# Performance work log

Measured on AMD Instinct MI355X. Metric: run time of the kernel, lower is better.

Reference implementation:

```python
import jax, jax.numpy as jnp
import numpy as np

B, C, M = 8192, 1024, 4096  # batch, controller width, memory_size


def setup_inputs() -> dict:
    key = jax.random.key(0)
    k1, k2, k3 = jax.random.split(key, 3)
    memory = jax.random.normal(k1, (B, M), dtype=jnp.float32)
    controller_output = jax.random.normal(k2, (B, C), dtype=jnp.float32)
    W = jax.random.normal(k3, (C, M), dtype=jnp.float32) * 0.02  # Dense kernel
    b = jnp.zeros((M,), dtype=jnp.float32)                       # Dense bias
    return {"memory": memory, "controller_output": controller_output, "W": W, "b": b}


def _l2_normalize(x, eps=1e-12):
    # matches tf.linalg.l2_normalize: x / sqrt(max(sum(x^2), eps))
    return x / jnp.sqrt(jnp.maximum(jnp.sum(x * x, axis=-1, keepdims=True), eps))


def reference(memory, controller_output, W, b):
    # Dense key projection followed by softmax over memory width
    key_vec = jax.nn.softmax(controller_output @ W + b, axis=-1)        # [B, M]
    # tf.keras.losses.cosine_similarity = -sum(l2n(a) * l2n(b), -1)
    sims = -jnp.sum(_l2_normalize(key_vec) * _l2_normalize(memory), axis=-1)  # [B]
    read_weights = jax.nn.softmax(sims, axis=-1)                        # softmax over B (as in source)
    read_vector = jnp.sum(read_weights[:, None] * memory, axis=1)       # [B]
    return read_vector
```

## Files before the change

kernel.cpp:

```cpp
#include <hip/hip_runtime.h>

#define NB 8192
#define NC 1024
#define NM 4096
#define NCH 16

typedef __attribute__((ext_vector_type(8))) short bf16x8;
typedef __attribute__((ext_vector_type(4))) float f32x4;

__device__ __forceinline__ unsigned short f2bf(float x) {
  unsigned int u = __float_as_uint(x);
  u += 0x7FFFu + ((u >> 16) & 1u);
  return (unsigned short)(u >> 16);
}
__device__ __forceinline__ float bf2f(unsigned short h) {
  return __uint_as_float(((unsigned int)h) << 16);
}
__device__ __forceinline__ unsigned int pk2(float a, float b) {
  return (unsigned int)f2bf(a) | ((unsigned int)f2bf(b) << 16);
}

__device__ __forceinline__ void gload_lds16(const void* g, void* l) {
  __builtin_amdgcn_global_load_lds(
      (const __attribute__((address_space(1))) unsigned int*)g,
      (__attribute__((address_space(3))) unsigned int*)l, 16, 0, 0);
}

#define DSR(dst, addr, IMM) \
  asm volatile("ds_read_b128 %0, %1 offset:" IMM : "=v"(dst) : "v"(addr))

#define BAR asm volatile("s_barrier" ::: "memory")
#define SBAR __builtin_amdgcn_sched_barrier(0)

__global__ __launch_bounds__(256) void prep_k(const float* __restrict__ W,
                                              unsigned short* __restrict__ Wt,
                                              const float* __restrict__ coin,
                                              unsigned short* __restrict__ Abf) {
  __shared__ float tile[64][65];
  const int bid = blockIdx.x;
  const int t = threadIdx.x;
  if (bid < 1024) {
    const int n0 = (bid & 63) * 64, k0 = (bid >> 6) * 64;
    const int r = t >> 2, q = t & 3;
    const float4* src = reinterpret_cast<const float4*>(W + (size_t)(k0 + r) * NM + n0 + q * 16);
    float4 x0 = src[0], x1 = src[1], x2 = src[2], x3 = src[3];
    float* tr = &tile[r][q * 16];
    tr[0]=x0.x; tr[1]=x0.y; tr[2]=x0.z;  tr[3]=x0.w;
    tr[4]=x1.x; tr[5]=x1.y; tr[6]=x1.z;  tr[7]=x1.w;
    tr[8]=x2.x; tr[9]=x2.y; tr[10]=x2.z; tr[11]=x2.w;
    tr[12]=x3.x; tr[13]=x3.y; tr[14]=x3.z; tr[15]=x3.w;
    __syncthreads();
    unsigned int pk[8];
#pragma unroll
    for (int i = 0; i < 8; ++i)
      pk[i] = pk2(tile[q * 16 + 2 * i][r], tile[q * 16 + 2 * i + 1][r]);
    int4* dst = reinterpret_cast<int4*>(Wt + (size_t)(n0 + r) * NC + k0 + q * 16);
    dst[0] = make_int4((int)pk[0], (int)pk[1], (int)pk[2], (int)pk[3]);
    dst[1] = make_int4((int)pk[4], (int)pk[5], (int)pk[6], (int)pk[7]);
  } else {
    const size_t i = ((size_t)(bid - 1024) * 256 + t) * 8;
    const float4* s = reinterpret_cast<const float4*>(coin + i);
    float4 x0 = s[0], x1 = s[1];
    int4 o = make_int4((int)pk2(x0.x, x0.y), (int)pk2(x0.z, x0.w),
                       (int)pk2(x1.x, x1.y), (int)pk2(x1.z, x1.w));
    *reinterpret_cast<int4*>(Abf + i) = o;
  }
}

__global__ __launch_bounds__(512) void gemm_fused(
    const unsigned short* __restrict__ Abf, const float* __restrict__ memry,
    const unsigned short* __restrict__ Wt, const float* __restrict__ bvec,
    float* __restrict__ pdotg, float* __restrict__ pesqg,
    float* __restrict__ pmsqg, float* __restrict__ pmsg) {
  __shared__ __align__(16) unsigned short LDS[2][4][8192];
  const int bm = blockIdx.x, bn = blockIdx.y;
  const int row0 = bm * 256, col0 = bn * 256;
  const int t = threadIdx.x;
  const int wid = t >> 6, lane = t & 63;
  const int wr = wid >> 2, wc = wid & 3;
  const int l15 = lane & 15, lg = lane >> 4;
  const int ga8 = (lg ^ ((l15 >> 1) & 3)) * 8;

  f32x4 acc[8][4];
#pragma unroll
  for (int mi = 0; mi < 8; ++mi)
#pragma unroll
    for (int ni = 0; ni < 4; ++ni) acc[mi][ni] = (f32x4){0.f, 0.f, 0.f, 0.f};

  const unsigned ldsbase =
      (unsigned)(uintptr_t)(__attribute__((address_space(3))) void*)&LDS[0][0][0];
  const unsigned abase = ldsbase + ((wr * 128 + l15) * 32 + ga8) * 2;
  const unsigned bbase = ldsbase + 32768 + ((wc * 64 + l15) * 32 + ga8) * 2;

  const int srow0 = t >> 2;
  const int sk8 = ((t & 3) ^ ((srow0 >> 1) & 3)) * 8;
  const unsigned short* gA = Abf + (size_t)(row0 + srow0) * NC + sk8;
  const unsigned short* gB = Wt + (size_t)(col0 + srow0) * NC + sk8;

#define STG(SL, TY, KT)                                                      \
  {                                                                          \
    const unsigned short* s0 = ((TY) <= 1 ? gA : gB) + (KT) * 64 + ((TY)&1) * 32; \
    gload_lds16(s0, &LDS[SL][TY][t * 8]);                                    \
    gload_lds16(s0 + (size_t)128 * NC, &LDS[SL][TY][t * 8 + 4096]);          \
  }
#define NOSTG
#define VM10 asm volatile("s_waitcnt vmcnt(10)" ::: "memory")
#define VM8 asm volatile("s_waitcnt vmcnt(8)" ::: "memory")
#define VM4 asm volatile("s_waitcnt vmcnt(4)" ::: "memory")
#define VM0 asm volatile("s_waitcnt vmcnt(0)" ::: "memory")
#define NOVM

#define MFMG(ACCH, MI, AMF, BMF)                                             \
  _Pragma("unroll") for (int ni = 0; ni < 4; ++ni)                           \
      acc[(ACCH)*4 + (MI)][ni] = __builtin_amdgcn_mfma_f32_16x16x32_bf16(    \
          AMF[MI], BMF[ni], acc[(ACCH)*4 + (MI)][ni], 0, 0, 0);

#define PH(ACCH, AMF, BMF, LDB, BLD, LDA, ALD, NSL, NS, NMH, STAGE, VM)      \
  {                                                                          \
    asm volatile("s_waitcnt lgkmcnt(0)" ::: "memory");                       \
    SBAR;                                                                    \
    __builtin_amdgcn_s_setprio(1);                                           \
    MFMG(ACCH, 0, AMF, BMF);                                                 \
    SBAR;                                                                    \
    if (LDB) {                                                               \
      const unsigned ba = bbase + (NSL)*65536 + (NS)*16384;                  \
      DSR(BLD[0], ba, "0");    DSR(BLD[1], ba, "1024");                      \
      DSR(BLD[2], ba, "2048"); DSR(BLD[3], ba, "3072");                      \
    }                                                                        \
    SBAR;                                                                    \
    MFMG(ACCH, 1, AMF, BMF);                                                 \
    SBAR;                                                                    \
    if (LDA) {                                                               \
      const unsigned aa = abase + (NSL)*65536 + (NS)*16384 + (NMH)*4096;     \
      DSR(ALD[0], aa, "0");    DSR(ALD[1], aa, "1024");                      \
      DSR(ALD[2], aa, "2048"); DSR(ALD[3], aa, "3072");                      \
    }                                                                        \
    SBAR;                                                                    \
    MFMG(ACCH, 2, AMF, BMF);                                                 \
    SBAR;                                                                    \
    STAGE;                                                                   \
    VM;                                                                      \
    SBAR;                                                                    \
    MFMG(ACCH, 3, AMF, BMF);                                                 \
    __builtin_amdgcn_s_setprio(0);                                           \
    BAR;                                                                     \
    SBAR;                                                                    \
  }

  STG(0, 2, 0); STG(0, 0, 0); STG(0, 3, 0); STG(0, 1, 0);
  STG(1, 2, 1); STG(1, 0, 1); STG(1, 3, 1);
  VM10;
  BAR;
  SBAR;

  bf16x8 aA[4], aB[4], bA[4], bB[4];
  {
    const unsigned ba = bbase;
    DSR(bA[0], ba, "0");    DSR(bA[1], ba, "1024");
    DSR(bA[2], ba, "2048"); DSR(bA[3], ba, "3072");
    const unsigned aa = abase;
    DSR(aA[0], aa, "0");    DSR(aA[1], aa, "1024");
    DSR(aA[2], aa, "2048"); DSR(aA[3], aa, "3072");
  }

  for (int it = 0; it < 7; ++it) {
    const int c1 = 2 * it + 1, c2 = 2 * it + 2, c3 = 2 * it + 3;
    PH(0, aA, bA, 0, bB, 1, aB, 0, 0, 1, STG(1, 1, c1), VM8);
    PH(1, aB, bA, 1, bB, 1, aA, 0, 1, 0, STG(0, 2, c2), NOVM);
    PH(0, aA, bB, 0, bA, 1, aB, 0, 1, 1, STG(0, 0, c2), VM8);
    PH(1, aB, bB, 1, bA, 1, aA, 1, 0, 0, STG(0, 3, c2), NOVM);
    PH(0, aA, bA, 0, bB, 1, aB, 1, 0, 1, STG(0, 1, c2), VM8);
    PH(1, aB, bA, 1, bB, 1, aA, 1, 1, 0, STG(1, 2, c3), NOVM);
    PH(0, aA, bB, 0, bA, 1, aB, 1, 1, 1, STG(1, 0, c3), VM8);
    PH(1, aB, bB, 1, bA, 1, aA, 0, 0, 0, STG(1, 3, c3), NOVM);
  }
  PH(0, aA, bA, 0, bB, 1, aB, 0, 0, 1, STG(1, 1, 15), VM8);
  PH(1, aB, bA, 1, bB, 1, aA, 0, 1, 0, NOSTG,         NOVM);
  PH(0, aA, bB, 0, bA, 1, aB, 0, 1, 1, NOSTG,         VM4);
  PH(1, aB, bB, 1, bA, 1, aA, 1, 0, 0, NOSTG,         NOVM);
  PH(0, aA, bA, 0, bB, 1, aB, 1, 0, 1, NOSTG,         VM0);
  PH(1, aB, bA, 1, bB, 1, aA, 1, 1, 0, NOSTG,         NOVM);
  PH(0, aA, bB, 0, bA, 1, aB, 1, 1, 1, NOSTG,         NOVM);
  PH(1, aB, bB, 0, bA, 0, aA, 0, 0, 0, NOSTG,         NOVM);
#undef PH
#undef MFMG
#undef STG

  asm volatile("s_waitcnt lgkmcnt(0)" ::: "memory");
  unsigned short (*e_lds)[256] = reinterpret_cast<unsigned short(*)[256]>(&LDS[0][0][0]);
  float bv[4];
#pragma unroll
  for (int ni = 0; ni < 4; ++ni) bv[ni] = bvec[col0 + wc * 64 + ni * 16 + l15];
#pragma unroll
  for (int mi = 0; mi < 8; ++mi)
#pragma unroll
    for (int ni = 0; ni < 4; ++ni)
#pragma unroll
      for (int j = 0; j < 4; ++j) {
        const int rl = wr * 128 + mi * 16 + 4 * lg + j;
        const int cl = wc * 64 + ni * 16 + l15;
        e_lds[rl][cl ^ (((rl >> 2) & 3) << 4)] = f2bf(__expf(acc[mi][ni][j] + bv[ni]));
      }
  __syncthreads();

  {
    const int halfl = lane >> 5, l31 = lane & 31;
    const int rbase = wid * 32;
#pragma unroll 8
    for (int i = 0; i < 16; ++i) {
      const int rl = rbase + 2 * i + halfl;
      const float4* mp = reinterpret_cast<const float4*>(
          memry + (size_t)(row0 + rl) * NM + col0 + l31 * 8);
      float4 m0 = mp[0], m1 = mp[1];
      bf16x8 ev = *reinterpret_cast<const bf16x8*>(
          &e_lds[rl][(l31 * 8) ^ (((rl >> 2) & 3) << 4)]);
      float mv[8] = {m0.x, m0.y, m0.z, m0.w, m1.x, m1.y, m1.z, m1.w};
      float pd = 0.f, pe = 0.f, pq = 0.f, pm = 0.f;
#pragma unroll
      for (int k = 0; k < 8; ++k) {
        float e = bf2f((unsigned short)ev[k]);
        pd += e * mv[k]; pe += e * e; pq += mv[k] * mv[k]; pm += mv[k];
      }
#pragma unroll
      for (int sh = 1; sh < 32; sh <<= 1) {
        pd += __shfl_xor(pd, sh); pe += __shfl_xor(pe, sh);
        pq += __shfl_xor(pq, sh); pm += __shfl_xor(pm, sh);
      }
      if (l31 == 0) {
        const int idx = (row0 + rl) * NCH + bn;
        pdotg[idx] = pd; pesqg[idx] = pe; pmsqg[idx] = pq; pmsg[idx] = pm;
      }
    }
  }
}

__global__ __launch_bounds__(256) void finalize_k(
    const float* __restrict__ pd, const float* __restrict__ pe,
    const float* __restrict__ pq, const float* __restrict__ pm,
    float* __restrict__ sims, float* __restrict__ mst) {
  const int r = blockIdx.x * 256 + threadIdx.x;
  float d = 0.f, e = 0.f, q = 0.f, m = 0.f;
#pragma unroll
  for (int i = 0; i < NCH; ++i) {
    d += pd[r * NCH + i];
    e += pe[r * NCH + i];
    q += pq[r * NCH + i];
    m += pm[r * NCH + i];
  }
  sims[r] = -d / (sqrtf(fmaxf(e, 1e-12f)) * sqrtf(fmaxf(q, 1e-12f)));
  mst[r] = m;
}

__global__ __launch_bounds__(1024) void softmax_out_k(
    const float* __restrict__ sims, const float* __restrict__ mst,
    float* __restrict__ out) {
  __shared__ float red[16];
  const int t = threadIdx.x;
  float v[8];
  float mx = -1e30f;
#pragma unroll
  for (int i = 0; i < 8; ++i) {
    v[i] = sims[t + i * 1024];
    mx = fmaxf(mx, v[i]);
  }
#pragma unroll
  for (int s = 1; s < 64; s <<= 1) mx = fmaxf(mx, __shfl_xor(mx, s));
  if ((t & 63) == 0) red[t >> 6] = mx;
  __syncthreads();
  float m2 = red[0];
#pragma unroll
  for (int i = 1; i < 16; ++i) m2 = fmaxf(m2, red[i]);
  mx = m2;
  float sum = 0.f;
#pragma unroll
  for (int i = 0; i < 8; ++i) sum += __expf(v[i] - mx);
#pragma unroll
  for (int s = 1; s < 64; s <<= 1) sum += __shfl_xor(sum, s);
  __syncthreads();
  if ((t & 63) == 0) red[t >> 6] = sum;
  __syncthreads();
  float s2 = 0.f;
#pragma unroll
  for (int i = 0; i < 16; ++i) s2 += red[i];
  const float inv = 1.0f / s2;
#pragma unroll
  for (int i = 0; i < 8; ++i)
    out[t + i * 1024] = __expf(v[i] - mx) * inv * mst[t + i * 1024];
}

extern "C" void kernel_launch(void* const* d_in, const int* in_sizes, int n_in,
                              void* d_out, int out_size, void* d_ws, size_t ws_size,
                              hipStream_t stream) {
  const float* memry = (const float*)d_in[0];
  const float* co    = (const float*)d_in[1];
  const float* W     = (const float*)d_in[2];
  const float* bvec  = (const float*)d_in[3];
  float* out = (float*)d_out;

  char* w = (char*)d_ws;
  unsigned short* Wt  = (unsigned short*)w;
  unsigned short* Abf = Wt + (size_t)NM * NC;
  float* pdot = (float*)(Abf + (size_t)NB * NC);
  float* pesq = pdot + (size_t)NB * NCH;
  float* pmsq = pesq + (size_t)NB * NCH;
  float* pms  = pmsq + (size_t)NB * NCH;
  float* sims = pms  + (size_t)NB * NCH;
  float* mst  = sims + NB;

  prep_k<<<1024 + (size_t)NB * NC / (256 * 8), 256, 0, stream>>>(W, Wt, co, Abf);
  gemm_fused<<<dim3(NB / 256, NM / 256), 512, 0, stream>>>(Abf, memry, Wt, bvec,
                                                           pdot, pesq, pmsq, pms);
  finalize_k<<<NB / 256, 256, 0, stream>>>(pdot, pesq, pmsq, pms, sims, mst);
  softmax_out_k<<<1, 1024, 0, stream>>>(sims, mst, out);
}
```

Baseline: 105.2 us.

## Restructure GEMM main loop into fused full-K-step phases with in-phase A reloads

Rewrites the software-pipelined MFMA main loop so that each phase covers both M-halves of one k-substep. The second A half is reloaded in place mid-phase, which frees the separate aB/bB register sets, and two global-to-LDS stages are issued per phase. Barriers and vmcnt waits drop from eight per two k-tiles to four, and the prologue and epilogue are reshuffled to match. This reduces barrier and wait overhead, but adds an LDS read plus lgkmcnt(0) stall inside each phase.

```diff
diff --git a/kernel.cpp b/kernel.cpp
--- a/kernel.cpp
+++ b/kernel.cpp
@@ -31,6 +31,7 @@
 
 #define BAR asm volatile("s_barrier" ::: "memory")
 #define SBAR __builtin_amdgcn_sched_barrier(0)
+#define LGKM0 asm volatile("s_waitcnt lgkmcnt(0)" ::: "memory")
 
 __global__ __launch_bounds__(256) void prep_k(const float* __restrict__ W,
                                               unsigned short* __restrict__ Wt,
@@ -104,89 +105,101 @@
     gload_lds16(s0 + (size_t)128 * NC, &LDS[SL][TY][t * 8 + 4096]);          \
   }
 #define NOSTG
-#define VM10 asm volatile("s_waitcnt vmcnt(10)" ::: "memory")
 #define VM8 asm volatile("s_waitcnt vmcnt(8)" ::: "memory")
 #define VM4 asm volatile("s_waitcnt vmcnt(4)" ::: "memory")
 #define VM0 asm volatile("s_waitcnt vmcnt(0)" ::: "memory")
 #define NOVM
 
-#define MFMG(ACCH, MI, AMF, BMF)                                             \
+#define MFMG0(UA, UB, MI)                                                    \
   _Pragma("unroll") for (int ni = 0; ni < 4; ++ni)                           \
-      acc[(ACCH)*4 + (MI)][ni] = __builtin_amdgcn_mfma_f32_16x16x32_bf16(    \
-          AMF[MI], BMF[ni], acc[(ACCH)*4 + (MI)][ni], 0, 0, 0);
-
-#define PH(ACCH, AMF, BMF, LDB, BLD, LDA, ALD, NSL, NS, NMH, STAGE, VM)      \
+      acc[MI][ni] = __builtin_amdgcn_mfma_f32_16x16x32_bf16(                 \
+          UA[MI], UB[ni], acc[MI][ni], 0, 0, 0);
+#define MFMG1(UA, UB, MI)                                                    \
+  _Pragma("unroll") for (int ni = 0; ni < 4; ++ni)                           \
+      acc[4 + (MI)][ni] = __builtin_amdgcn_mfma_f32_16x16x32_bf16(           \
+          UA[MI], UB[ni], acc[4 + (MI)][ni], 0, 0, 0);
+
+#define PH(UA, UB, VA, VB, DOREAD, NSL, NS, CSL, CS, STG1, STG2, VM)         \
   {                                                                          \
-    asm volatile("s_waitcnt lgkmcnt(0)" ::: "memory");                       \
+    LGKM0;                                                                   \
     SBAR;                                                                    \
     __builtin_amdgcn_s_setprio(1);                                           \
-    MFMG(ACCH, 0, AMF, BMF);                                                 \
-    SBAR;                                                                    \
-    if (LDB) {                                                               \
+    MFMG0(UA, UB, 0);                                                        \
+    SBAR;                                                                    \
+    if (DOREAD) {                                                            \
       const unsigned ba = bbase + (NSL)*65536 + (NS)*16384;                  \
-      DSR(BLD[0], ba, "0");    DSR(BLD[1], ba, "1024");                      \
-      DSR(BLD[2], ba, "2048"); DSR(BLD[3], ba, "3072");                      \
+      DSR(VB[0], ba, "0");    DSR(VB[1], ba, "1024");                        \
+      DSR(VB[2], ba, "2048"); DSR(VB[3], ba, "3072");                        \
     }                                                                        \
     SBAR;                                                                    \
-    MFMG(ACCH, 1, AMF, BMF);                                                 \
-    SBAR;                                                                    \
-    if (LDA) {                                                               \
-      const unsigned aa = abase + (NSL)*65536 + (NS)*16384 + (NMH)*4096;     \
-      DSR(ALD[0], aa, "0");    DSR(ALD[1], aa, "1024");                      \
-      DSR(ALD[2], aa, "2048"); DSR(ALD[3], aa, "3072");                      \
+    MFMG0(UA, UB, 1);                                                        \
+    SBAR;                                                                    \
+    if (DOREAD) {                                                            \
+      const unsigned aa = abase + (NSL)*65536 + (NS)*16384;                  \
+      DSR(VA[0], aa, "0");    DSR(VA[1], aa, "1024");                        \
+      DSR(VA[2], aa, "2048"); DSR(VA[3], aa, "3072");                        \
     }                                                                        \
     SBAR;                                                                    \
-    MFMG(ACCH, 2, AMF, BMF);                                                 \
-    SBAR;                                                                    \
-    STAGE;                                                                   \
+    MFMG0(UA, UB, 2);                                                        \
+    SBAR;                                                                    \
+    STG1;                                                                    \
+    SBAR;                                                                    \
+    MFMG0(UA, UB, 3);                                                        \
+    SBAR;                                                                    \
+    {                                                                        \
+      const unsigned ca = abase + (CSL)*65536 + (CS)*16384 + 4096;           \
+      DSR(UA[0], ca, "0");    DSR(UA[1], ca, "1024");                        \
+      DSR(UA[2], ca, "2048"); DSR(UA[3], ca, "3072");                        \
+    }                                                                        \
+    SBAR;                                                                    \
+    LGKM0;                                                                   \
+    SBAR;                                                                    \
+    MFMG1(UA, UB, 0);                                                        \
+    SBAR;                                                                    \
+    STG2;                                                                    \
+    SBAR;                                                                    \
+    MFMG1(UA, UB, 1);                                                        \
+    SBAR;                                                                    \
     VM;                                                                      \
     SBAR;                                                                    \
-    MFMG(ACCH, 3, AMF, BMF);                                                 \
+    MFMG1(UA, UB, 2);                                                        \
+    MFMG1(UA, UB, 3);                                                        \
     __builtin_amdgcn_s_setprio(0);                                           \
     BAR;                                                                     \
     SBAR;                                                                    \
   }
 
-  STG(0, 2, 0); STG(0, 0, 0); STG(0, 3, 0); STG(0, 1, 0);
-  STG(1, 2, 1); STG(1, 0, 1); STG(1, 3, 1);
-  VM10;
+  STG(0, 0, 0); STG(0, 2, 0); STG(0, 1, 0); STG(0, 3, 0);
+  STG(1, 0, 1); STG(1, 2, 1); STG(1, 1, 1); STG(1, 3, 1);
+  VM8;
   BAR;
   SBAR;
 
-  bf16x8 aA[4], aB[4], bA[4], bB[4];
+  bf16x8 xA[4], xB[4], yA[4], yB[4];
   {
-    const unsigned ba = bbase;
-    DSR(bA[0], ba, "0");    DSR(bA[1], ba, "1024");
-    DSR(bA[2], ba, "2048"); DSR(bA[3], ba, "3072");
-    const unsigned aa = abase;
-    DSR(aA[0], aa, "0");    DSR(aA[1], aa, "1024");
-    DSR(aA[2], aa, "2048"); DSR(aA[3], aa, "3072");
-  }
-
+    DSR(xB[0], bbase, "0");    DSR(xB[1], bbase, "1024");
+    DSR(xB[2], bbase, "2048"); DSR(xB[3], bbase, "3072");
+    DSR(xA[0], abase, "0");    DSR(xA[1], abase, "1024");
+    DSR(xA[2], abase, "2048"); DSR(xA[3], abase, "3072");
+  }
+
+  PH(xA, xB, yA, yB, 1, 0, 1, 0, 0, NOSTG, NOSTG, VM4);
   for (int it = 0; it < 7; ++it) {
-    const int c1 = 2 * it + 1, c2 = 2 * it + 2, c3 = 2 * it + 3;
-    PH(0, aA, bA, 0, bB, 1, aB, 0, 0, 1, STG(1, 1, c1), VM8);
-    PH(1, aB, bA, 1, bB, 1, aA, 0, 1, 0, STG(0, 2, c2), NOVM);
-    PH(0, aA, bB, 0, bA, 1, aB, 0, 1, 1, STG(0, 0, c2), VM8);
-    PH(1, aB, bB, 1, bA, 1, aA, 1, 0, 0, STG(0, 3, c2), NOVM);
-    PH(0, aA, bA, 0, bB, 1, aB, 1, 0, 1, STG(0, 1, c2), VM8);
-    PH(1, aB, bA, 1, bB, 1, aA, 1, 1, 0, STG(1, 2, c3), NOVM);
-    PH(0, aA, bB, 0, bA, 1, aB, 1, 1, 1, STG(1, 0, c3), VM8);
-    PH(1, aB, bB, 1, bA, 1, aA, 0, 0, 0, STG(1, 3, c3), NOVM);
-  }
-  PH(0, aA, bA, 0, bB, 1, aB, 0, 0, 1, STG(1, 1, 15), VM8);
-  PH(1, aB, bA, 1, bB, 1, aA, 0, 1, 0, NOSTG,         NOVM);
-  PH(0, aA, bB, 0, bA, 1, aB, 0, 1, 1, NOSTG,         VM4);
-  PH(1, aB, bB, 1, bA, 1, aA, 1, 0, 0, NOSTG,         NOVM);
-  PH(0, aA, bA, 0, bB, 1, aB, 1, 0, 1, NOSTG,         VM0);
-  PH(1, aB, bA, 1, bB, 1, aA, 1, 1, 0, NOSTG,         NOVM);
-  PH(0, aA, bB, 0, bA, 1, aB, 1, 1, 1, NOSTG,         NOVM);
-  PH(1, aB, bB, 0, bA, 0, aA, 0, 0, 0, NOSTG,         NOVM);
+    const int c2 = 2 * it + 2, c3 = 2 * it + 3;
+    PH(yA, yB, xA, xB, 1, 1, 0, 0, 1, STG(0, 0, c2), STG(0, 2, c2), VM4);
+    PH(xA, xB, yA, yB, 1, 1, 1, 1, 0, STG(0, 1, c2), STG(0, 3, c2), VM4);
+    PH(yA, yB, xA, xB, 1, 0, 0, 1, 1, STG(1, 0, c3), STG(1, 2, c3), VM4);
+    PH(xA, xB, yA, yB, 1, 0, 1, 0, 0, STG(1, 1, c3), STG(1, 3, c3), VM4);
+  }
+  PH(yA, yB, xA, xB, 1, 1, 0, 0, 1, NOSTG, NOSTG, VM0);
+  PH(xA, xB, yA, yB, 1, 1, 1, 1, 0, NOSTG, NOSTG, NOVM);
+  PH(yA, yB, xA, xB, 0, 0, 0, 1, 1, NOSTG, NOSTG, NOVM);
 #undef PH
-#undef MFMG
+#undef MFMG0
+#undef MFMG1
 #undef STG
 
-  asm volatile("s_waitcnt lgkmcnt(0)" ::: "memory");
+  LGKM0;
   unsigned short (*e_lds)[256] = reinterpret_cast<unsigned short(*)[256]>(&LDS[0][0][0]);
   float bv[4];
 #pragma unroll
```

New measurement: 103.9 us, median of 2. Within noise of the previous version (-1.2%).
